# Optimization experiments

Measured on AMD Instinct MI355X. Metric: run time of the kernel, lower is better.

The kernel has to match this reference:

```python
import jax, jax.numpy as jnp
import numpy as np

B = 131072   # batch of states (e.g. ODE integrator batch)
S = 2        # state_dim (q, p)
H = 512      # hidden_dim
E = 8        # action_embedding_dim


def setup_inputs() -> dict:
    key = jax.random.key(0)
    ks = jax.random.split(key, 8)
    sc = lambda n: 1.0 / np.sqrt(n)
    return {
        "t": 0,  # unused time scalar (odeint signature)
        "state": jax.random.normal(ks[0], (B, S), dtype=jnp.float32),
        "action_emb": jax.random.normal(ks[1], (B, E), dtype=jnp.float32),
        # H_net: Linear(S,H) -> Softplus -> Linear(H,H) -> Softplus -> Linear(H,1)
        "W1": jax.random.normal(ks[2], (S, H), dtype=jnp.float32) * sc(S),
        "b1": jnp.zeros((H,), dtype=jnp.float32),
        "W2": jax.random.normal(ks[3], (H, H), dtype=jnp.float32) * sc(H),
        "b2": jnp.zeros((H,), dtype=jnp.float32),
        "W3": jax.random.normal(ks[4], (H, 1), dtype=jnp.float32) * sc(H),
        "b3": jnp.zeros((1,), dtype=jnp.float32),
        "log_damping": jnp.asarray(-1.0, dtype=jnp.float32),
        # G_net: Linear(E, S//2)
        "Gw": jax.random.normal(ks[5], (E, S // 2), dtype=jnp.float32) * sc(E),
        "Gb": jnp.zeros((S // 2,), dtype=jnp.float32),
    }


def reference(t, state, action_emb, W1, b1, W2, b2, W3, b3, log_damping, Gw, Gb):
    # Hamiltonian net: scalar H per state; sum over batch so jax.grad gives
    # per-sample dH/dstate in one pass (equivalent to autograd.grad with ones cotangent).
    def H_sum(s):
        h = jax.nn.softplus(s @ W1 + b1)       # [B, H]
        h = jax.nn.softplus(h @ W2 + b2)       # [B, H]
        return jnp.sum(h @ W3 + b3)            # scalar

    dH_dstate = jax.grad(H_sum)(state)         # [B, S]
    dH_dq = dH_dstate[..., 0:1]                # [B, 1]
    dH_dp = dH_dstate[..., 1:2]                # [B, 1]

    damping = jnp.exp(log_damping)
    G_u = action_emb @ Gw + Gb                 # [B, 1]

    dq_dt = dH_dp
    dp_dt = -dH_dq - damping * dH_dp + G_u
    return jnp.concatenate([dq_dt, dp_dt], axis=-1)  # [B, S]
```

## Files before the change

kernel.cpp:

```cpp
#include <hip/hip_runtime.h>

typedef __bf16 bf16x8 __attribute__((ext_vector_type(8)));
typedef float f32x4 __attribute__((ext_vector_type(4)));
typedef float f32x16 __attribute__((ext_vector_type(16)));
typedef unsigned short u16x8 __attribute__((ext_vector_type(8)));

#define DEVI static __device__ __forceinline__

DEVI unsigned short f2b(float x) {
  __bf16 b = (__bf16)x;
  return __builtin_bit_cast(unsigned short, b);
}

DEVI float ex2(float x) {
#if __has_builtin(__builtin_amdgcn_exp2f)
  return __builtin_amdgcn_exp2f(x);
#else
  return __expf(x * 0.69314718f);
#endif
}
DEVI float lg2(float x) {
#if __has_builtin(__builtin_amdgcn_logf)
  return __builtin_amdgcn_logf(x);
#else
  return __logf(x) * 1.44269504f;
#endif
}

__global__ __launch_bounds__(256) void pack_w2_kernel(
    const float* __restrict__ W2, unsigned short* __restrict__ p1,
    unsigned short* __restrict__ p2) {
  int idx = blockIdx.x * 256 + threadIdx.x;
  int which = idx >> 18;
  int i = idx & 262143;
  int j = i & 7;
  int l = (i >> 3) & 63;
  if (which == 0) {
    int t0 = (i >> 9) & 15;
    int s = i >> 13;
    p1[i] = f2b(W2[(s * 16 + (l >> 5) * 8 + j) * 512 + t0 * 32 + (l & 31)]);
  } else {
    int t0 = (i >> 9) & 31;
    int s = i >> 14;
    p2[i] = f2b(W2[(t0 * 16 + (l & 15)) * 512 + s * 32 + (l >> 4) * 8 + j]);
  }
}

__global__ __launch_bounds__(512, 4) void phm_kernel(
    const float* __restrict__ state, const float* __restrict__ action_emb,
    const float* __restrict__ W1, const float* __restrict__ b1,
    const float* __restrict__ b2, const float* __restrict__ W3,
    const float* __restrict__ log_damping, const float* __restrict__ Gw,
    const float* __restrict__ Gb, const unsigned short* __restrict__ packB1,
    const unsigned short* __restrict__ packB2, float* __restrict__ out) {
  __shared__ unsigned short buf[64 * 512];
  __shared__ float W1s[1024];
  __shared__ float b1s[512];
  __shared__ float b2s[512];
  __shared__ float W3s[512];
  __shared__ float st[128];
  __shared__ float2 part2[8][64];

  const int t = threadIdx.x;
  const int lane = t & 63;
  const int wid = t >> 6;
  const int l15 = lane & 15;
  const int l4 = lane >> 4;
  const int l31 = lane & 31;
  const int l5 = lane >> 5;
  const long row0 = (long)blockIdx.x * 64;
  char* bufc = reinterpret_cast<char*>(buf);
  const float LOG2E = 1.44269504f;

  for (int i = t; i < 512; i += 512) {
    W1s[i] = W1[i] * LOG2E;
    W1s[512 + i] = W1[512 + i] * LOG2E;
    b1s[i] = b1[i] * LOG2E;
    b2s[i] = b2[i] * LOG2E;
    W3s[i] = W3[i];
  }
  if (t < 128) st[t] = state[row0 * 2 + t];
  __syncthreads();

#pragma unroll
  for (int it = 0; it < 8; ++it) {
    int page = it * 8 + wid;
    int s = page >> 1, rt = page & 1;
    int row = rt * 32 + l31;
    int k0 = s * 16 + l5 * 8;
    float s0 = st[row * 2], s1 = st[row * 2 + 1];
    u16x8 pk;
#pragma unroll
    for (int j = 0; j < 8; ++j) {
      int c = k0 + j;
      float zp = fmaf(s0, W1s[c], fmaf(s1, W1s[512 + c], b1s[c]));
      float hp = fmaxf(zp, 0.f) + lg2(1.f + ex2(-fabsf(zp)));
      pk[j] = f2b(hp);
    }
    *reinterpret_cast<u16x8*>(bufc + page * 1024 + lane * 16) = pk;
  }
  __syncthreads();

  f32x16 acc1[2][2];
#pragma unroll
  for (int rt = 0; rt < 2; ++rt)
#pragma unroll
    for (int ct = 0; ct < 2; ++ct)
#pragma unroll
      for (int r = 0; r < 16; ++r) acc1[rt][ct][r] = 0.f;

#pragma unroll 2
  for (int s = 0; s < 32; ++s) {
    bf16x8 af[2];
#pragma unroll
    for (int rt = 0; rt < 2; ++rt)
      af[rt] = __builtin_bit_cast(
          bf16x8, *reinterpret_cast<const int4*>(
                      bufc + (s * 2 + rt) * 1024 + lane * 16));
    bf16x8 bfr[2];
#pragma unroll
    for (int ct = 0; ct < 2; ++ct)
      bfr[ct] = __builtin_bit_cast(
          bf16x8, *reinterpret_cast<const int4*>(
                      packB1 + ((s * 16 + wid * 2 + ct) * 64 + lane) * 8));
#pragma unroll
    for (int rt = 0; rt < 2; ++rt)
#pragma unroll
      for (int ct = 0; ct < 2; ++ct)
        acc1[rt][ct] = __builtin_amdgcn_mfma_f32_32x32x16_bf16(
            af[rt], bfr[ct], acc1[rt][ct], 0, 0, 0);
  }
  __syncthreads();

#pragma unroll
  for (int ct = 0; ct < 2; ++ct) {
    int c = (wid * 2 + ct) * 32 + l31;
    float w3 = W3s[c], bbL = b2s[c];
    int pbase = (c >> 5) * 4096 + (c & 7) * 2;
    int oct = (c >> 3) & 3;
#pragma unroll
    for (int rt = 0; rt < 2; ++rt) {
#pragma unroll
      for (int reg = 0; reg < 16; ++reg) {
        int row = rt * 32 + (reg & 3) + 8 * (reg >> 2) + 4 * l5;
        float e = ex2(-(acc1[rt][ct][reg] + bbL));
        float sg = __builtin_amdgcn_rcpf(1.f + e);
        unsigned short u = f2b(w3 * sg);
        int lane2 = (row & 15) + 16 * oct;
        int slot = lane2 ^ (lane2 >> 4);
        *reinterpret_cast<unsigned short*>(
            bufc + pbase + (row >> 4) * 1024 + slot * 16) = u;
      }
    }
  }
  __syncthreads();

  float p0[16], p1v[16];
#pragma unroll
  for (int i = 0; i < 16; ++i) { p0[i] = 0.f; p1v[i] = 0.f; }

  const int rslot = (lane ^ (lane >> 4)) * 16;
#pragma unroll
  for (int chunk = 0; chunk < 2; ++chunk) {
    f32x4 acc2[4][2];
#pragma unroll
    for (int a = 0; a < 4; ++a)
#pragma unroll
      for (int b = 0; b < 2; ++b)
#pragma unroll
        for (int r = 0; r < 4; ++r) acc2[a][b][r] = 0.f;

#pragma unroll 2
    for (int s2 = 0; s2 < 16; ++s2) {
      bf16x8 af[4];
#pragma unroll
      for (int rt2 = 0; rt2 < 4; ++rt2)
        af[rt2] = __builtin_bit_cast(
            bf16x8, *reinterpret_cast<const int4*>(
                        bufc + s2 * 4096 + rt2 * 1024 + rslot));
      bf16x8 bfr[2];
#pragma unroll
      for (int cc = 0; cc < 2; ++cc)
        bfr[cc] = __builtin_bit_cast(
            bf16x8,
            *reinterpret_cast<const int4*>(
                packB2 + ((s2 * 32 + wid * 4 + chunk * 2 + cc) * 64 + lane) * 8));
#pragma unroll
      for (int rt2 = 0; rt2 < 4; ++rt2)
#pragma unroll
        for (int cc = 0; cc < 2; ++cc)
          acc2[rt2][cc] = __builtin_amdgcn_mfma_f32_16x16x32_bf16(
              af[rt2], bfr[cc], acc2[rt2][cc], 0, 0, 0);
    }
#pragma unroll
    for (int rt2 = 0; rt2 < 4; ++rt2) {
      float2 rv[4];
#pragma unroll
      for (int jj = 0; jj < 4; ++jj)
        rv[jj] = *reinterpret_cast<const float2*>(
            &st[(rt2 * 16 + l4 * 4 + jj) * 2]);
#pragma unroll
      for (int cc = 0; cc < 2; ++cc) {
        int hc = wid * 64 + (chunk * 2 + cc) * 16 + l15;
        float w10L = W1s[hc], w11L = W1s[512 + hc], bbL = b1s[hc];
#pragma unroll
        for (int jj = 0; jj < 4; ++jj) {
          float z1L = fmaf(rv[jj].x, w10L, fmaf(rv[jj].y, w11L, bbL));
          float sg = __builtin_amdgcn_rcpf(1.f + ex2(-z1L));
          float dz1 = acc2[rt2][cc][jj] * sg;
          p0[rt2 * 4 + jj] = fmaf(dz1, w10L, p0[rt2 * 4 + jj]);
          p1v[rt2 * 4 + jj] = fmaf(dz1, w11L, p1v[rt2 * 4 + jj]);
        }
      }
    }
  }

  float a8[8], b8[8];
  {
    bool bb = (l15 & 1) != 0;
#pragma unroll
    for (int m = 0; m < 8; ++m) {
      float ka = bb ? p0[2 * m + 1] : p0[2 * m];
      float sa = bb ? p0[2 * m] : p0[2 * m + 1];
      a8[m] = ka + __shfl_xor(sa, 1, 64);
      float kb = bb ? p1v[2 * m + 1] : p1v[2 * m];
      float sb = bb ? p1v[2 * m] : p1v[2 * m + 1];
      b8[m] = kb + __shfl_xor(sb, 1, 64);
    }
  }
  float a4[4], b4[4];
  {
    bool bb = (l15 & 2) != 0;
#pragma unroll
    for (int m = 0; m < 4; ++m) {
      float ka = bb ? a8[2 * m + 1] : a8[2 * m];
      float sa = bb ? a8[2 * m] : a8[2 * m + 1];
      a4[m] = ka + __shfl_xor(sa, 2, 64);
      float kb = bb ? b8[2 * m + 1] : b8[2 * m];
      float sb = bb ? b8[2 * m] : b8[2 * m + 1];
      b4[m] = kb + __shfl_xor(sb, 2, 64);
    }
  }
  float a2[2], b2v[2];
  {
    bool bb = (l15 & 4) != 0;
#pragma unroll
    for (int m = 0; m < 2; ++m) {
      float ka = bb ? a4[2 * m + 1] : a4[2 * m];
      float sa = bb ? a4[2 * m] : a4[2 * m + 1];
      a2[m] = ka + __shfl_xor(sa, 4, 64);
      float kb = bb ? b4[2 * m + 1] : b4[2 * m];
      float sb = bb ? b4[2 * m] : b4[2 * m + 1];
      b2v[m] = kb + __shfl_xor(sb, 4, 64);
    }
  }
  float a1, b1r;
  {
    bool bb = (l15 & 8) != 0;
    float ka = bb ? a2[1] : a2[0];
    float sa = bb ? a2[0] : a2[1];
    a1 = ka + __shfl_xor(sa, 8, 64);
    float kb = bb ? b2v[1] : b2v[0];
    float sb = bb ? b2v[0] : b2v[1];
    b1r = kb + __shfl_xor(sb, 8, 64);
  }
  {
    int r = (l15 >> 2) * 16 + l4 * 4 + (l15 & 3);
    part2[wid][r] = make_float2(a1, b1r);
  }
  __syncthreads();

  if (t < 64) {
    long grow = row0 + t;
    float g0 = 0.f, g1 = 0.f;
#pragma unroll
    for (int w = 0; w < 8; ++w) {
      float2 pp = part2[w][t];
      g0 += pp.x;
      g1 += pp.y;
    }
    const float LN2 = 0.69314718f;
    g0 *= LN2;
    g1 *= LN2;
    const float4 ae0 = reinterpret_cast<const float4*>(action_emb)[grow * 2];
    const float4 ae1 = reinterpret_cast<const float4*>(action_emb)[grow * 2 + 1];
    float gu = Gb[0];
    gu = fmaf(ae0.x, Gw[0], gu);
    gu = fmaf(ae0.y, Gw[1], gu);
    gu = fmaf(ae0.z, Gw[2], gu);
    gu = fmaf(ae0.w, Gw[3], gu);
    gu = fmaf(ae1.x, Gw[4], gu);
    gu = fmaf(ae1.y, Gw[5], gu);
    gu = fmaf(ae1.z, Gw[6], gu);
    gu = fmaf(ae1.w, Gw[7], gu);
    float damping = __expf(log_damping[0]);
    float2 o;
    o.x = g1;
    o.y = -g0 - damping * g1 + gu;
    reinterpret_cast<float2*>(out)[grow] = o;
  }
}

extern "C" void kernel_launch(void* const* d_in, const int* in_sizes, int n_in,
                              void* d_out, int out_size, void* d_ws,
                              size_t ws_size, hipStream_t stream) {
  const float* state = (const float*)d_in[1];
  const float* action_emb = (const float*)d_in[2];
  const float* W1 = (const float*)d_in[3];
  const float* b1 = (const float*)d_in[4];
  const float* W2 = (const float*)d_in[5];
  const float* b2 = (const float*)d_in[6];
  const float* W3 = (const float*)d_in[7];
  const float* log_damping = (const float*)d_in[9];
  const float* Gw = (const float*)d_in[10];
  const float* Gb = (const float*)d_in[11];
  float* out = (float*)d_out;

  unsigned short* p1 = (unsigned short*)d_ws;
  unsigned short* p2 = p1 + 262144;

  pack_w2_kernel<<<dim3(2048), dim3(256), 0, stream>>>(W2, p1, p2);
  phm_kernel<<<dim3(2048), dim3(512), 0, stream>>>(
      state, action_emb, W1, b1, b2, W3, log_damping, Gw, Gb, p1, p2, out);
}
```

Baseline: 155.2 us.

## Double rows per block to 128 with 16 waves to halve weight reloads

Each block now processes 128 rows with 1024 threads instead of 64 rows with 512 threads, and the grid is halved. In the first GEMM each wave owns one 32-column slice across four row tiles, so each packed W2 fragment feeds four MFMAs. In the backward GEMM the waves split into two row halves, which halves total global/L2 traffic for the packed weights. The cost is double the LDS per block (about 128KB for the activation buffer), which limits blocks per CU and may reduce occupancy and latency hiding.

```diff
diff --git a/kernel.cpp b/kernel.cpp
--- a/kernel.cpp
+++ b/kernel.cpp
@@ -46,20 +46,20 @@
   }
 }
 
-__global__ __launch_bounds__(512, 4) void phm_kernel(
+__global__ __launch_bounds__(1024, 4) void phm_kernel(
     const float* __restrict__ state, const float* __restrict__ action_emb,
     const float* __restrict__ W1, const float* __restrict__ b1,
     const float* __restrict__ b2, const float* __restrict__ W3,
     const float* __restrict__ log_damping, const float* __restrict__ Gw,
     const float* __restrict__ Gb, const unsigned short* __restrict__ packB1,
     const unsigned short* __restrict__ packB2, float* __restrict__ out) {
-  __shared__ unsigned short buf[64 * 512];
+  __shared__ unsigned short buf[128 * 512];
   __shared__ float W1s[1024];
   __shared__ float b1s[512];
   __shared__ float b2s[512];
   __shared__ float W3s[512];
-  __shared__ float st[128];
-  __shared__ float2 part2[8][64];
+  __shared__ float st[256];
+  __shared__ float2 part2[16][64];
 
   const int t = threadIdx.x;
   const int lane = t & 63;
@@ -68,24 +68,24 @@
   const int l4 = lane >> 4;
   const int l31 = lane & 31;
   const int l5 = lane >> 5;
-  const long row0 = (long)blockIdx.x * 64;
+  const long row0 = (long)blockIdx.x * 128;
   char* bufc = reinterpret_cast<char*>(buf);
   const float LOG2E = 1.44269504f;
 
-  for (int i = t; i < 512; i += 512) {
-    W1s[i] = W1[i] * LOG2E;
-    W1s[512 + i] = W1[512 + i] * LOG2E;
-    b1s[i] = b1[i] * LOG2E;
-    b2s[i] = b2[i] * LOG2E;
-    W3s[i] = W3[i];
-  }
-  if (t < 128) st[t] = state[row0 * 2 + t];
+  if (t < 512) {
+    W1s[t] = W1[t] * LOG2E;
+    W1s[512 + t] = W1[512 + t] * LOG2E;
+    b1s[t] = b1[t] * LOG2E;
+    b2s[t] = b2[t] * LOG2E;
+    W3s[t] = W3[t];
+  }
+  if (t < 256) st[t] = state[row0 * 2 + t];
   __syncthreads();
 
 #pragma unroll
   for (int it = 0; it < 8; ++it) {
-    int page = it * 8 + wid;
-    int s = page >> 1, rt = page & 1;
+    int page = it * 16 + wid;
+    int s = page >> 2, rt = page & 3;
     int row = rt * 32 + l31;
     int k0 = s * 16 + l5 * 8;
     float s0 = st[row * 2], s1 = st[row * 2 + 1];
@@ -101,49 +101,39 @@
   }
   __syncthreads();
 
-  f32x16 acc1[2][2];
-#pragma unroll
-  for (int rt = 0; rt < 2; ++rt)
-#pragma unroll
-    for (int ct = 0; ct < 2; ++ct)
-#pragma unroll
-      for (int r = 0; r < 16; ++r) acc1[rt][ct][r] = 0.f;
+  f32x16 acc1[4];
+#pragma unroll
+  for (int rt = 0; rt < 4; ++rt)
+#pragma unroll
+    for (int r = 0; r < 16; ++r) acc1[rt][r] = 0.f;
 
 #pragma unroll 2
   for (int s = 0; s < 32; ++s) {
-    bf16x8 af[2];
-#pragma unroll
-    for (int rt = 0; rt < 2; ++rt)
-      af[rt] = __builtin_bit_cast(
+    bf16x8 bfr = __builtin_bit_cast(
+        bf16x8, *reinterpret_cast<const int4*>(
+                    packB1 + ((s * 16 + wid) * 64 + lane) * 8));
+#pragma unroll
+    for (int rt = 0; rt < 4; ++rt) {
+      bf16x8 af = __builtin_bit_cast(
           bf16x8, *reinterpret_cast<const int4*>(
-                      bufc + (s * 2 + rt) * 1024 + lane * 16));
-    bf16x8 bfr[2];
-#pragma unroll
-    for (int ct = 0; ct < 2; ++ct)
-      bfr[ct] = __builtin_bit_cast(
-          bf16x8, *reinterpret_cast<const int4*>(
-                      packB1 + ((s * 16 + wid * 2 + ct) * 64 + lane) * 8));
-#pragma unroll
-    for (int rt = 0; rt < 2; ++rt)
-#pragma unroll
-      for (int ct = 0; ct < 2; ++ct)
-        acc1[rt][ct] = __builtin_amdgcn_mfma_f32_32x32x16_bf16(
-            af[rt], bfr[ct], acc1[rt][ct], 0, 0, 0);
-  }
-  __syncthreads();
-
-#pragma unroll
-  for (int ct = 0; ct < 2; ++ct) {
-    int c = (wid * 2 + ct) * 32 + l31;
+                      bufc + (s * 4 + rt) * 1024 + lane * 16));
+      acc1[rt] = __builtin_amdgcn_mfma_f32_32x32x16_bf16(
+          af, bfr, acc1[rt], 0, 0, 0);
+    }
+  }
+  __syncthreads();
+
+  {
+    int c = wid * 32 + l31;
     float w3 = W3s[c], bbL = b2s[c];
-    int pbase = (c >> 5) * 4096 + (c & 7) * 2;
+    int pbase = (c >> 5) * 8192 + (c & 7) * 2;
     int oct = (c >> 3) & 3;
 #pragma unroll
-    for (int rt = 0; rt < 2; ++rt) {
+    for (int rt = 0; rt < 4; ++rt) {
 #pragma unroll
       for (int reg = 0; reg < 16; ++reg) {
         int row = rt * 32 + (reg & 3) + 8 * (reg >> 2) + 4 * l5;
-        float e = ex2(-(acc1[rt][ct][reg] + bbL));
+        float e = ex2(-(acc1[rt][reg] + bbL));
         float sg = __builtin_amdgcn_rcpf(1.f + e);
         unsigned short u = f2b(w3 * sg);
         int lane2 = (row & 15) + 16 * oct;
@@ -155,6 +145,8 @@
   }
   __syncthreads();
 
+  const int rh = wid >> 3;
+  const int cs = wid & 7;
   float p0[16], p1v[16];
 #pragma unroll
   for (int i = 0; i < 16; ++i) { p0[i] = 0.f; p1v[i] = 0.f; }
@@ -177,14 +169,15 @@
       for (int rt2 = 0; rt2 < 4; ++rt2)
         af[rt2] = __builtin_bit_cast(
             bf16x8, *reinterpret_cast<const int4*>(
-                        bufc + s2 * 4096 + rt2 * 1024 + rslot));
+                        bufc + (s2 * 8 + rh * 4 + rt2) * 1024 + rslot));
       bf16x8 bfr[2];
 #pragma unroll
       for (int cc = 0; cc < 2; ++cc)
         bfr[cc] = __builtin_bit_cast(
             bf16x8,
             *reinterpret_cast<const int4*>(
-                packB2 + ((s2 * 32 + wid * 4 + chunk * 2 + cc) * 64 + lane) * 8));
+                packB2 +
+                ((s2 * 32 + cs * 4 + chunk * 2 + cc) * 64 + lane) * 8));
 #pragma unroll
       for (int rt2 = 0; rt2 < 4; ++rt2)
 #pragma unroll
@@ -198,10 +191,10 @@
 #pragma unroll
       for (int jj = 0; jj < 4; ++jj)
         rv[jj] = *reinterpret_cast<const float2*>(
-            &st[(rt2 * 16 + l4 * 4 + jj) * 2]);
+            &st[(rh * 64 + rt2 * 16 + l4 * 4 + jj) * 2]);
 #pragma unroll
       for (int cc = 0; cc < 2; ++cc) {
-        int hc = wid * 64 + (chunk * 2 + cc) * 16 + l15;
+        int hc = cs * 64 + (chunk * 2 + cc) * 16 + l15;
         float w10L = W1s[hc], w11L = W1s[512 + hc], bbL = b1s[hc];
 #pragma unroll
         for (int jj = 0; jj < 4; ++jj) {
@@ -270,12 +263,14 @@
   }
   __syncthreads();
 
-  if (t < 64) {
+  if (t < 128) {
     long grow = row0 + t;
+    int rhh = t >> 6;
+    int rl = t & 63;
     float g0 = 0.f, g1 = 0.f;
 #pragma unroll
     for (int w = 0; w < 8; ++w) {
-      float2 pp = part2[w][t];
+      float2 pp = part2[rhh * 8 + w][rl];
       g0 += pp.x;
       g1 += pp.y;
     }
@@ -320,6 +315,6 @@
   unsigned short* p2 = p1 + 262144;
 
   pack_w2_kernel<<<dim3(2048), dim3(256), 0, stream>>>(W2, p1, p2);
-  phm_kernel<<<dim3(2048), dim3(512), 0, stream>>>(
+  phm_kernel<<<dim3(1024), dim3(1024), 0, stream>>>(
       state, action_emb, W1, b1, b2, W3, log_damping, Gw, Gb, p1, p2, out);
 }
```

Measured after the change: 167.2 us. 1.08x slower.

## Switch backward GEMM to 32x32x16 MFMA with row-half/column-quarter wave split

Applied to the files above, without the earlier changes.

The second (backward) GEMM moves from 16x16x32 MFMAs, where each wave covered all 64 rows, to 32x32x16 MFMAs. Each wave now takes one 32-row half and a quarter of the hidden columns. The W2 packing layout, the shared-memory layout of the softplus-derivative activations, and the final cross-wave reduction are all changed to match. The goal is fewer A-fragment LDS reads per MFMA and fewer instructions per unit of work. In exchange it needs an extra shuffle-xor reduction step and a different register accumulator shape.

```diff
diff --git a/kernel.cpp b/kernel.cpp
--- a/kernel.cpp
+++ b/kernel.cpp
@@ -35,14 +35,12 @@
   int i = idx & 262143;
   int j = i & 7;
   int l = (i >> 3) & 63;
+  int t0 = (i >> 9) & 15;
+  int s = i >> 13;
   if (which == 0) {
-    int t0 = (i >> 9) & 15;
-    int s = i >> 13;
     p1[i] = f2b(W2[(s * 16 + (l >> 5) * 8 + j) * 512 + t0 * 32 + (l & 31)]);
   } else {
-    int t0 = (i >> 9) & 31;
-    int s = i >> 14;
-    p2[i] = f2b(W2[(t0 * 16 + (l & 15)) * 512 + s * 32 + (l >> 4) * 8 + j]);
+    p2[i] = f2b(W2[(t0 * 32 + (l & 31)) * 512 + s * 16 + (l >> 5) * 8 + j]);
   }
 }
 
@@ -59,13 +57,12 @@
   __shared__ float b2s[512];
   __shared__ float W3s[512];
   __shared__ float st[128];
-  __shared__ float2 part2[8][64];
+  __shared__ float2 part2[8][32];
 
   const int t = threadIdx.x;
   const int lane = t & 63;
   const int wid = t >> 6;
   const int l15 = lane & 15;
-  const int l4 = lane >> 4;
   const int l31 = lane & 31;
   const int l5 = lane >> 5;
   const long row0 = (long)blockIdx.x * 64;
@@ -136,25 +133,27 @@
   for (int ct = 0; ct < 2; ++ct) {
     int c = (wid * 2 + ct) * 32 + l31;
     float w3 = W3s[c], bbL = b2s[c];
-    int pbase = (c >> 5) * 4096 + (c & 7) * 2;
-    int oct = (c >> 3) & 3;
+    int pb = (c >> 4) * 2048 + (c & 7) * 2;
+    int chalf = (c >> 3) & 1;
 #pragma unroll
     for (int rt = 0; rt < 2; ++rt) {
 #pragma unroll
       for (int reg = 0; reg < 16; ++reg) {
-        int row = rt * 32 + (reg & 3) + 8 * (reg >> 2) + 4 * l5;
+        int row31 = (reg & 3) + 8 * (reg >> 2) + 4 * l5;
         float e = ex2(-(acc1[rt][ct][reg] + bbL));
         float sg = __builtin_amdgcn_rcpf(1.f + e);
         unsigned short u = f2b(w3 * sg);
-        int lane2 = (row & 15) + 16 * oct;
+        int lane2 = row31 + 32 * chalf;
         int slot = lane2 ^ (lane2 >> 4);
         *reinterpret_cast<unsigned short*>(
-            bufc + pbase + (row >> 4) * 1024 + slot * 16) = u;
+            bufc + pb + rt * 1024 + slot * 16) = u;
       }
     }
   }
   __syncthreads();
 
+  const int rh = wid >> 2;
+  const int cs = wid & 3;
   float p0[16], p1v[16];
 #pragma unroll
   for (int i = 0; i < 16; ++i) { p0[i] = 0.f; p1v[i] = 0.f; }
@@ -162,55 +161,44 @@
   const int rslot = (lane ^ (lane >> 4)) * 16;
 #pragma unroll
   for (int chunk = 0; chunk < 2; ++chunk) {
-    f32x4 acc2[4][2];
-#pragma unroll
-    for (int a = 0; a < 4; ++a)
-#pragma unroll
-      for (int b = 0; b < 2; ++b)
-#pragma unroll
-        for (int r = 0; r < 4; ++r) acc2[a][b][r] = 0.f;
+    f32x16 acc2[2];
+#pragma unroll
+    for (int cc = 0; cc < 2; ++cc)
+#pragma unroll
+      for (int r = 0; r < 16; ++r) acc2[cc][r] = 0.f;
 
 #pragma unroll 2
-    for (int s2 = 0; s2 < 16; ++s2) {
-      bf16x8 af[4];
-#pragma unroll
-      for (int rt2 = 0; rt2 < 4; ++rt2)
-        af[rt2] = __builtin_bit_cast(
-            bf16x8, *reinterpret_cast<const int4*>(
-                        bufc + s2 * 4096 + rt2 * 1024 + rslot));
+    for (int s2 = 0; s2 < 32; ++s2) {
+      bf16x8 af = __builtin_bit_cast(
+          bf16x8, *reinterpret_cast<const int4*>(
+                      bufc + (s2 * 2 + rh) * 1024 + rslot));
       bf16x8 bfr[2];
 #pragma unroll
       for (int cc = 0; cc < 2; ++cc)
         bfr[cc] = __builtin_bit_cast(
             bf16x8,
             *reinterpret_cast<const int4*>(
-                packB2 + ((s2 * 32 + wid * 4 + chunk * 2 + cc) * 64 + lane) * 8));
-#pragma unroll
-      for (int rt2 = 0; rt2 < 4; ++rt2)
-#pragma unroll
-        for (int cc = 0; cc < 2; ++cc)
-          acc2[rt2][cc] = __builtin_amdgcn_mfma_f32_16x16x32_bf16(
-              af[rt2], bfr[cc], acc2[rt2][cc], 0, 0, 0);
-    }
-#pragma unroll
-    for (int rt2 = 0; rt2 < 4; ++rt2) {
-      float2 rv[4];
-#pragma unroll
-      for (int jj = 0; jj < 4; ++jj)
-        rv[jj] = *reinterpret_cast<const float2*>(
-            &st[(rt2 * 16 + l4 * 4 + jj) * 2]);
-#pragma unroll
-      for (int cc = 0; cc < 2; ++cc) {
-        int hc = wid * 64 + (chunk * 2 + cc) * 16 + l15;
-        float w10L = W1s[hc], w11L = W1s[512 + hc], bbL = b1s[hc];
-#pragma unroll
-        for (int jj = 0; jj < 4; ++jj) {
-          float z1L = fmaf(rv[jj].x, w10L, fmaf(rv[jj].y, w11L, bbL));
-          float sg = __builtin_amdgcn_rcpf(1.f + ex2(-z1L));
-          float dz1 = acc2[rt2][cc][jj] * sg;
-          p0[rt2 * 4 + jj] = fmaf(dz1, w10L, p0[rt2 * 4 + jj]);
-          p1v[rt2 * 4 + jj] = fmaf(dz1, w11L, p1v[rt2 * 4 + jj]);
-        }
+                packB2 +
+                ((s2 * 16 + cs * 4 + chunk * 2 + cc) * 64 + lane) * 8));
+#pragma unroll
+      for (int cc = 0; cc < 2; ++cc)
+        acc2[cc] = __builtin_amdgcn_mfma_f32_32x32x16_bf16(
+            af, bfr[cc], acc2[cc], 0, 0, 0);
+    }
+#pragma unroll
+    for (int cc = 0; cc < 2; ++cc) {
+      int hc = cs * 128 + (chunk * 2 + cc) * 32 + l31;
+      float w10L = W1s[hc], w11L = W1s[512 + hc], bbL = b1s[hc];
+#pragma unroll
+      for (int reg = 0; reg < 16; ++reg) {
+        int rl32 = (reg & 3) + 8 * (reg >> 2) + 4 * l5;
+        float2 sp = *reinterpret_cast<const float2*>(
+            &st[(rh * 32 + rl32) * 2]);
+        float z1L = fmaf(sp.x, w10L, fmaf(sp.y, w11L, bbL));
+        float sg = __builtin_amdgcn_rcpf(1.f + ex2(-z1L));
+        float dz1 = acc2[cc][reg] * sg;
+        p0[reg] = fmaf(dz1, w10L, p0[reg]);
+        p1v[reg] = fmaf(dz1, w11L, p1v[reg]);
       }
     }
   }
@@ -264,18 +252,22 @@
     float sb = bb ? b2v[0] : b2v[1];
     b1r = kb + __shfl_xor(sb, 8, 64);
   }
-  {
-    int r = (l15 >> 2) * 16 + l4 * 4 + (l15 & 3);
-    part2[wid][r] = make_float2(a1, b1r);
+  a1 += __shfl_xor(a1, 16, 64);
+  b1r += __shfl_xor(b1r, 16, 64);
+  if ((lane & 16) == 0) {
+    int r32 = (l15 & 3) + 8 * (l15 >> 2) + 4 * l5;
+    part2[wid][r32] = make_float2(a1, b1r);
   }
   __syncthreads();
 
   if (t < 64) {
     long grow = row0 + t;
+    int rhh = t >> 5;
+    int rl = t & 31;
     float g0 = 0.f, g1 = 0.f;
 #pragma unroll
-    for (int w = 0; w < 8; ++w) {
-      float2 pp = part2[w][t];
+    for (int w = 0; w < 4; ++w) {
+      float2 pp = part2[rhh * 4 + w][rl];
       g0 += pp.x;
       g1 += pp.y;
     }
```

Measured after the change: 228.1 us. 47.0% more time.
